# Optimization experiments

Measured on AMD Instinct MI355X. Metric: run time of the kernel, lower is better.

## Reference

```python
import jax, jax.numpy as jnp
import numpy as np

# Mex config (matches init_kwargs)
B, C, H, W = 64, 64, 64, 64
BLK = (64, 3, 3)        # block over (C, H, W); spans all channels -> out_c = 1
STR = (64, 2, 2)
PAD = (0, 1, 1)
NI = 256                # num_instances
EPS = 1.0
SOFTMAX_MODE = False    # False -> mean (logsumexp - log k), True -> plain logsumexp


def setup_inputs() -> dict:
    key = jax.random.key(0)
    k1, k2 = jax.random.split(key)
    x = jax.random.normal(k1, (B, C, H, W), dtype=jnp.float32)
    kblk = BLK[0] * BLK[1] * BLK[2]
    # Dirichlet([1]*k) init == normalized exponentials; nregions = 1 (shared offsets)
    e = jax.random.exponential(k2, (1, NI, kblk), dtype=jnp.float32)
    offsets = (e / jnp.sum(e, axis=-1, keepdims=True)).reshape(1, NI, *BLK)
    return {"x": x, "offsets": offsets}


def _mex_forward(x, offsets):
    eps = jnp.float32(EPS)
    bc, bh, bw = BLK
    # im2col patch extraction: (B, C*bh*bw, OH, OW); feature dim ordered (c, fh, fw)
    patches = jax.lax.conv_general_dilated_patches(
        x, (bh, bw), (STR[1], STR[2]),
        [(PAD[1], PAD[1]), (PAD[2], PAD[2])],  # zero padding == blocks_out_of_bounds_value
        dimension_numbers=("NCHW", "OIHW", "NCHW"),
    )
    Bn, K, OH, OW = patches.shape  # K = bc*bh*bw = 576
    P = patches.transpose(0, 2, 3, 1).reshape(-1, K)  # (N, k), N = B*OH*OW
    O = offsets.reshape(NI, K)                         # single shared region

    # y_ni = (1/eps) * logsumexp_k( eps*(P_nk + O_ik) ) - log(k)/eps (mean mode)
    # exp-domain GEMM with max-shift for stability:
    Pe = eps * P
    Oe = eps * O
    mp = jnp.max(Pe, axis=1, keepdims=True)   # (N, 1)
    mo = jnp.max(Oe, axis=1, keepdims=True)   # (I, 1)
    S = jnp.exp(Pe - mp) @ jnp.exp(Oe - mo).T  # (N, I)
    y = (jnp.log(S) + mp + mo.T) / eps
    if not SOFTMAX_MODE:
        y = y - jnp.log(jnp.float32(K)) / eps
    # output: (B, num_instances * out_c, OH, OW) with out_c = 1
    return y.reshape(Bn, OH, OW, NI).transpose(0, 3, 1, 2)


def reference(x, offsets):
    return _mex_forward(x, offsets)
```

## Files before the change

### kernel.cpp

```cpp
#include <hip/hip_runtime.h>
#include <hip/hip_bf16.h>


typedef __bf16 bf16x8 __attribute__((ext_vector_type(8)));
typedef float  f32x4  __attribute__((ext_vector_type(4)));

#define GLD16(gp, lp) __builtin_amdgcn_global_load_lds(                        \
    (const __attribute__((address_space(1))) unsigned int*)(gp),               \
    (__attribute__((address_space(3))) unsigned int*)(lp), 16, 0, 0)

__global__ void mex_prep_b(const float* __restrict__ off, __bf16* __restrict__ Bt) {
    const int i = blockIdx.x * 4 + (threadIdx.x >> 6);
    const int c = threadIdx.x & 63;
    const float* oi = off + i * 576;
    __bf16* bi = Bt + i * 576;
    #pragma unroll
    for (int p = 0; p < 9; ++p) {
        float v = oi[c * 9 + p];
        bi[p * 64 + c] = (__bf16)__expf(v);
    }
}

__global__ __launch_bounds__(256) void mex_exp_tr(const float* __restrict__ x,
                                                  __bf16* __restrict__ E) {
    __shared__ __bf16 t[64 * 68];
    const int bh = blockIdx.x;
    const int b  = bh >> 6, h = bh & 63;
    const float* xp = x + ((size_t)b << 18) + (h << 6);
    const int tid = threadIdx.x;

    #pragma unroll
    for (int i = 0; i < 4; ++i) {
        const int f  = tid + i * 256;
        const int c  = f >> 4;
        const int w0 = (f & 15) << 2;
        float4 v = *(const float4*)(xp + c * 4096 + w0);
        __bf16* d = &t[c * 68 + w0];
        d[0] = (__bf16)__expf(v.x);
        d[1] = (__bf16)__expf(v.y);
        d[2] = (__bf16)__expf(v.z);
        d[3] = (__bf16)__expf(v.w);
    }
    __syncthreads();

    __bf16* Erow = E + ((size_t)bh << 12);
    #pragma unroll
    for (int j = 0; j < 2; ++j) {
        const int id = tid + j * 256;
        const int w = id >> 3, c8 = id & 7;
        bf16x8 v;
        #pragma unroll
        for (int ii = 0; ii < 8; ++ii) v[ii] = t[(c8 * 8 + ii) * 68 + w];
        const int c8p = c8 ^ ((w >> 1) & 7);
        *(bf16x8*)(Erow + w * 64 + c8p * 8) = v;
    }
}

__global__ __launch_bounds__(256, 3) void mex_main(
        const __bf16* __restrict__ E,
        const __bf16* __restrict__ Bt,
        float* __restrict__ out) {
    __shared__ bf16x8 lds8[5 * 66 * 8];

    const int bid = blockIdx.x;
    const int b   = bid >> 4;
    const int oh0 = (bid & 15) << 1;
    const int tid  = threadIdx.x;
    const int lane = tid & 63;
    const int wv   = tid >> 6;

    bf16x8 one8;
    #pragma unroll
    for (int j = 0; j < 8; ++j) one8[j] = (__bf16)1.0f;
    if (tid < 40) {
        const int hl = tid >> 3, cc = tid & 7;
        lds8[(hl * 66) * 8 + cc] = one8;
    }
    if (oh0 == 0) {
        for (int i = tid; i < 66 * 8; i += 256) lds8[i] = one8;
    }

    #pragma unroll
    for (int s = 0; s < 10; ++s) {
        const int seg = wv * 10 + s;
        const int hl = seg >> 3, sg = seg & 7;
        const int hg = 2 * oh0 - 1 + hl;
        if (hg >= 0) {
            const __bf16* gp = E + (((size_t)b * 64 + hg) << 12) + (sg << 9) + (lane << 3);
            bf16x8* lp = lds8 + hl * 528 + 8 + sg * 64;
            GLD16(gp, lp);
        }
    }
    __syncthreads();

    const int t16 = tid & 15;
    const int q   = (tid >> 4) & 3;

    int rbase[4], owv[4];
    #pragma unroll
    for (int mt = 0; mt < 4; ++mt) {
        const int m = mt * 16 + t16;
        owv[mt]   = m & 31;
        rbase[mt] = ((m >> 5) * 132) + ((m & 31) * 2);
    }

    const bf16x8* __restrict__ Btv = (const bf16x8*)Bt;
    const int instRow = (wv * 64 + t16) * 72 + q;

    f32x4 acc[4][4];
    #pragma unroll
    for (int mt = 0; mt < 4; ++mt)
        #pragma unroll
        for (int nt = 0; nt < 4; ++nt)
            acc[mt][nt] = (f32x4)(0.0f);

    bf16x8 bcur[4];
    #pragma unroll
    for (int nt = 0; nt < 4; ++nt)
        bcur[nt] = Btv[instRow + nt * (16 * 72)];

    #pragma unroll 2
    for (int ks = 0; ks < 18; ++ks) {
        const int p  = ks >> 1;
        const int fh = (p * 11) >> 5;
        const int fw = p - fh * 3;
        const int rofs = fh * 66 + fw;
        const int ccq  = ((ks & 1) << 2) + q;

        bf16x8 a[4];
        #pragma unroll
        for (int mt = 0; mt < 4; ++mt) {
            const int row = rbase[mt] + rofs;
            const int key = ((owv[mt] * 2 + fw - 1) >> 1) & 7;
            a[mt] = lds8[row * 8 + (ccq ^ key)];
        }

        bf16x8 bnext[4];
        if (ks < 17) {
            #pragma unroll
            for (int nt = 0; nt < 4; ++nt)
                bnext[nt] = Btv[instRow + nt * (16 * 72) + (ks + 1) * 4];
        }

        #pragma unroll
        for (int mt = 0; mt < 4; ++mt)
            #pragma unroll
            for (int nt = 0; nt < 4; ++nt)
                acc[mt][nt] = __builtin_amdgcn_mfma_f32_16x16x32_bf16(
                    a[mt], bcur[nt], acc[mt][nt], 0, 0, 0);

        #pragma unroll
        for (int nt = 0; nt < 4; ++nt) bcur[nt] = bnext[nt];
    }

    const float lK = 6.356107660695891f;
    #pragma unroll
    for (int mt = 0; mt < 4; ++mt) {
        const int m   = mt * 16 + (q << 2);
        const int ohl = m >> 5;
        const int owi = m & 31;
        const int orow = (oh0 + ohl) * 32 + owi;
        #pragma unroll
        for (int nt = 0; nt < 4; ++nt) {
            const int inst = wv * 64 + nt * 16 + t16;
            f32x4 r;
            #pragma unroll
            for (int j = 0; j < 4; ++j)
                r[j] = __logf(acc[mt][nt][j]) - lK;
            *(f32x4*)(out + (((size_t)b * 256 + inst) * 1024 + orow)) = r;
        }
    }
}

extern "C" void kernel_launch(void* const* d_in, const int* in_sizes, int n_in,
                              void* d_out, int out_size, void* d_ws, size_t ws_size,
                              hipStream_t stream) {
    const float* x   = (const float*)d_in[0];
    const float* off = (const float*)d_in[1];
    float* out = (float*)d_out;
    __bf16* E  = (__bf16*)d_ws;
    __bf16* Bt = (__bf16*)((char*)d_ws + 33554432);

    mex_prep_b<<<64, 256, 0, stream>>>(off, Bt);
    mex_exp_tr<<<4096, 256, 0, stream>>>(x, E);
    mex_main<<<1024, 256, 0, stream>>>(E, Bt, out);
}
```

Before: 156.7 us.

## Fuse exp/transpose of input into main GEMM kernel, dropping intermediate buffer

Removes the separate kernel that exponentiated and transposed x into a bf16 workspace. The main kernel now reads fp32 x directly, applies exp, converts to bf16 and writes swizzled rows into LDS. This eliminates a 32MB intermediate write and read plus a kernel launch. In exchange, overlapping halo rows are exponentiated redundantly, and the async global-to-LDS loads are replaced by register-staged loads.

Measured after the change: 155.9 us. No clear change (-0.5%).

```diff
diff --git a/kernel.cpp b/kernel.cpp
--- a/kernel.cpp
+++ b/kernel.cpp
@@ -4,10 +4,6 @@
 
 typedef __bf16 bf16x8 __attribute__((ext_vector_type(8)));
 typedef float  f32x4  __attribute__((ext_vector_type(4)));
-
-#define GLD16(gp, lp) __builtin_amdgcn_global_load_lds(                        \
-    (const __attribute__((address_space(1))) unsigned int*)(gp),               \
-    (__attribute__((address_space(3))) unsigned int*)(lp), 16, 0, 0)
 
 __global__ void mex_prep_b(const float* __restrict__ off, __bf16* __restrict__ Bt) {
     const int i = blockIdx.x * 4 + (threadIdx.x >> 6);
@@ -21,43 +17,8 @@
     }
 }
 
-__global__ __launch_bounds__(256) void mex_exp_tr(const float* __restrict__ x,
-                                                  __bf16* __restrict__ E) {
-    __shared__ __bf16 t[64 * 68];
-    const int bh = blockIdx.x;
-    const int b  = bh >> 6, h = bh & 63;
-    const float* xp = x + ((size_t)b << 18) + (h << 6);
-    const int tid = threadIdx.x;
-
-    #pragma unroll
-    for (int i = 0; i < 4; ++i) {
-        const int f  = tid + i * 256;
-        const int c  = f >> 4;
-        const int w0 = (f & 15) << 2;
-        float4 v = *(const float4*)(xp + c * 4096 + w0);
-        __bf16* d = &t[c * 68 + w0];
-        d[0] = (__bf16)__expf(v.x);
-        d[1] = (__bf16)__expf(v.y);
-        d[2] = (__bf16)__expf(v.z);
-        d[3] = (__bf16)__expf(v.w);
-    }
-    __syncthreads();
-
-    __bf16* Erow = E + ((size_t)bh << 12);
-    #pragma unroll
-    for (int j = 0; j < 2; ++j) {
-        const int id = tid + j * 256;
-        const int w = id >> 3, c8 = id & 7;
-        bf16x8 v;
-        #pragma unroll
-        for (int ii = 0; ii < 8; ++ii) v[ii] = t[(c8 * 8 + ii) * 68 + w];
-        const int c8p = c8 ^ ((w >> 1) & 7);
-        *(bf16x8*)(Erow + w * 64 + c8p * 8) = v;
-    }
-}
-
 __global__ __launch_bounds__(256, 3) void mex_main(
-        const __bf16* __restrict__ E,
+        const float* __restrict__ x,
         const __bf16* __restrict__ Bt,
         float* __restrict__ out) {
     __shared__ bf16x8 lds8[5 * 66 * 8];
@@ -66,7 +27,6 @@
     const int b   = bid >> 4;
     const int oh0 = (bid & 15) << 1;
     const int tid  = threadIdx.x;
-    const int lane = tid & 63;
     const int wv   = tid >> 6;
 
     bf16x8 one8;
@@ -80,15 +40,31 @@
         for (int i = tid; i < 66 * 8; i += 256) lds8[i] = one8;
     }
 
-    #pragma unroll
-    for (int s = 0; s < 10; ++s) {
-        const int seg = wv * 10 + s;
-        const int hl = seg >> 3, sg = seg & 7;
-        const int hg = 2 * oh0 - 1 + hl;
-        if (hg >= 0) {
-            const __bf16* gp = E + (((size_t)b * 64 + hg) << 12) + (sg << 9) + (lane << 3);
-            bf16x8* lp = lds8 + hl * 528 + 8 + sg * 64;
-            GLD16(gp, lp);
+    {
+        const int wp  = tid & 31;
+        const int w0  = wp << 1;
+        const int c8  = tid >> 5;
+        const int c8p = c8 ^ (wp & 7);
+        const float* xb = x + ((size_t)b << 18) + w0;
+        #pragma unroll
+        for (int hl = 0; hl < 5; ++hl) {
+            const int hg = 2 * oh0 - 1 + hl;
+            if (hg >= 0) {
+                const float* xp = xb + (hg << 6);
+                float2 v[8];
+                #pragma unroll
+                for (int k = 0; k < 8; ++k)
+                    v[k] = *(const float2*)(xp + (((c8 << 3) + k) << 12));
+                bf16x8 ca, cb;
+                #pragma unroll
+                for (int k = 0; k < 8; ++k) {
+                    ca[k] = (__bf16)__expf(v[k].x);
+                    cb[k] = (__bf16)__expf(v[k].y);
+                }
+                bf16x8* dst = lds8 + hl * 528 + (w0 + 1) * 8 + c8p;
+                dst[0] = ca;
+                dst[8] = cb;
+            }
         }
     }
     __syncthreads();
@@ -178,10 +154,8 @@
     const float* x   = (const float*)d_in[0];
     const float* off = (const float*)d_in[1];
     float* out = (float*)d_out;
-    __bf16* E  = (__bf16*)d_ws;
-    __bf16* Bt = (__bf16*)((char*)d_ws + 33554432);
+    __bf16* Bt = (__bf16*)d_ws;
 
     mex_prep_b<<<64, 256, 0, stream>>>(off, Bt);
-    mex_exp_tr<<<4096, 256, 0, stream>>>(x, E);
-    mex_main<<<1024, 256, 0, stream>>>(E, Bt, out);
+    mex_main<<<1024, 256, 0, stream>>>(x, Bt, out);
 }
```
